# Kernel tuning notes

Measured on AMD Instinct MI355X. Metric: run time of the kernel, lower is better.

The kernel has to match this reference:

```python
import jax, jax.numpy as jnp
import numpy as np

B, C, N = 2, 32, 1_000_000
V = 262_144  # num_voxels (64^3 grid)


def setup_inputs() -> dict:
    key = jax.random.key(0)
    kf, ki = jax.random.split(key)
    features = jax.random.normal(kf, (B, C, N), dtype=jnp.float32)
    indices = jax.random.randint(ki, (N,), 0, V, dtype=jnp.int32)
    return {"features": features, "indices": indices, "num_voxels": V}


def reference(features, indices, num_voxels):
    # voxelize: scatter-mean over irregular cluster indices (dim=2)
    b, c, n = features.shape
    sums = jnp.zeros((b, c, num_voxels), dtype=features.dtype).at[:, :, indices].add(features)
    counts = jnp.zeros((num_voxels,), dtype=features.dtype).at[indices].add(1.0)
    voxels = sums / jnp.maximum(counts, 1.0)  # [B, C, V]; empty voxels -> 0
    # devoxelize: gather voxel features back to points via the same index buffer
    points_out = voxels[:, :, indices]  # [B, C, N]
    return points_out
```

## Files before the change

### kernel.cpp

```cpp
#include <hip/hip_runtime.h>


constexpr int BC  = 64;
constexpr int VOX = 262144;
constexpr int SCAN_BLK = 1024;
constexpr int NSB = VOX / SCAN_BLK;
constexpr int RV  = 128;

__global__ __launch_bounds__(256) void hist_kernel(
    const int* __restrict__ idx, int* __restrict__ cursor, int N)
{
    int t = blockIdx.x * 256 + threadIdx.x;
    int n0 = t * 4;
    if (n0 >= N) return;
    int4 vi = *(const int4*)(idx + n0);
    atomicAdd(&cursor[vi.x], 1);
    atomicAdd(&cursor[vi.y], 1);
    atomicAdd(&cursor[vi.z], 1);
    atomicAdd(&cursor[vi.w], 1);
}

__global__ __launch_bounds__(256) void scan_blocks(
    int* __restrict__ cursor, int* __restrict__ partials)
{
    __shared__ int sm[256];
    int t = threadIdx.x, b = blockIdx.x;
    int base = b * SCAN_BLK + t * 4;
    int4 c = *(const int4*)(cursor + base);
    int s = c.x + c.y + c.z + c.w;
    sm[t] = s;
    __syncthreads();
    #pragma unroll
    for (int off = 1; off < 256; off <<= 1) {
        int add = (t >= off) ? sm[t - off] : 0;
        __syncthreads();
        sm[t] += add;
        __syncthreads();
    }
    int excl = sm[t] - s;
    int4 o;
    o.x = excl; o.y = excl + c.x; o.z = o.y + c.y; o.w = o.z + c.z;
    *(int4*)(cursor + base) = o;
    if (t == 255) partials[b] = sm[255];
}

__global__ __launch_bounds__(256) void scan_partials(int* __restrict__ partials)
{
    __shared__ int sm[256];
    int t = threadIdx.x;
    int v = partials[t];
    sm[t] = v;
    __syncthreads();
    #pragma unroll
    for (int off = 1; off < 256; off <<= 1) {
        int add = (t >= off) ? sm[t - off] : 0;
        __syncthreads();
        sm[t] += add;
        __syncthreads();
    }
    partials[t] = sm[t] - v;
}

__global__ __launch_bounds__(256) void scan_add(
    int* __restrict__ cursor, const int* __restrict__ partials)
{
    int t = blockIdx.x * 256 + threadIdx.x;
    int base = t * 4;
    int add = partials[base >> 10];
    int4 c = *(int4*)(cursor + base);
    c.x += add; c.y += add; c.z += add; c.w += add;
    *(int4*)(cursor + base) = c;
}

__global__ __launch_bounds__(256) void permute_scatter(
    const float* __restrict__ feat, const int* __restrict__ idx,
    int* __restrict__ cursor, float* __restrict__ sorted, int N)
{
    int p = blockIdx.x * 256 + threadIdx.x;
    if (p >= N) return;
    int v = idx[p];
    int j = atomicAdd(&cursor[v], 1);
    float* dst = sorted + (size_t)j * BC;

    #pragma unroll
    for (int c0 = 0; c0 < BC; c0 += 16) {
        float f[16];
        #pragma unroll
        for (int k = 0; k < 16; ++k)
            f[k] = feat[(size_t)(c0 + k) * N + p];
        #pragma unroll
        for (int q = 0; q < 4; ++q)
            *(float4*)(dst + c0 + 4 * q) =
                make_float4(f[4*q], f[4*q+1], f[4*q+2], f[4*q+3]);
    }
}

__global__ __launch_bounds__(256) void reduce_mean(
    const float* __restrict__ sorted, const int* __restrict__ cursor,
    float* __restrict__ mean)
{
    int t = threadIdx.x;
    int vL = t & (RV - 1);
    int half = t >> 7;
    int v = blockIdx.x * RV + vL;

    int end = cursor[v];
    int start = (v > 0) ? cursor[v - 1] : 0;
    float inv = 1.0f / fmaxf((float)(end - start), 1.0f);

    float4 acc[8] = {};
    for (int j = start; j < end; ++j) {
        const float4* row = (const float4*)(sorted + (size_t)j * BC) + half * 8;
        #pragma unroll
        for (int q = 0; q < 8; ++q) {
            float4 r = row[q];
            acc[q].x += r.x; acc[q].y += r.y; acc[q].z += r.z; acc[q].w += r.w;
        }
    }
    float* dst = mean + (size_t)v * BC + half * 32;
    #pragma unroll
    for (int q = 0; q < 8; ++q) {
        float4 o = make_float4(acc[q].x * inv, acc[q].y * inv,
                               acc[q].z * inv, acc[q].w * inv);
        *(float4*)(dst + 4 * q) = o;
    }
}

__global__ __launch_bounds__(256) void voxel_gather(
    const float* __restrict__ mean, const int* __restrict__ idx,
    float* __restrict__ out, int N)
{
    int p = blockIdx.x * 256 + threadIdx.x;
    if (p >= N) return;
    int v = idx[p];
    const float4* row = (const float4*)(mean + (size_t)v * BC);
    #pragma unroll
    for (int q = 0; q < 16; ++q) {
        float4 r = row[q];
        __builtin_nontemporal_store(r.x, &out[(size_t)(4 * q + 0) * N + p]);
        __builtin_nontemporal_store(r.y, &out[(size_t)(4 * q + 1) * N + p]);
        __builtin_nontemporal_store(r.z, &out[(size_t)(4 * q + 2) * N + p]);
        __builtin_nontemporal_store(r.w, &out[(size_t)(4 * q + 3) * N + p]);
    }
}

extern "C" void kernel_launch(void* const* d_in, const int* in_sizes, int n_in,
                              void* d_out, int out_size, void* d_ws, size_t ws_size,
                              hipStream_t stream) {
    const float* feat = (const float*)d_in[0];
    const int* idx = (const int*)d_in[1];
    float* out = (float*)d_out;
    int N = in_sizes[1];

    float* mean = (float*)d_ws;
    int* cursor = (int*)((char*)d_ws + (size_t)VOX * BC * 4);
    int* partials = (int*)d_ws;
    float* sorted = (float*)d_out;

    hipMemsetAsync(cursor, 0, (size_t)VOX * sizeof(int), stream);

    int pblocks4 = ((N + 3) / 4 + 255) / 256;
    int pblocks1 = (N + 255) / 256;

    hist_kernel    <<<pblocks4, 256, 0, stream>>>(idx, cursor, N);
    scan_blocks    <<<NSB, 256, 0, stream>>>(cursor, partials);
    scan_partials  <<<1, 256, 0, stream>>>(partials);
    scan_add       <<<VOX / SCAN_BLK, 256, 0, stream>>>(cursor, partials);
    permute_scatter<<<pblocks1, 256, 0, stream>>>(feat, idx, cursor, sorted, N);
    reduce_mean    <<<VOX / RV, 256, 0, stream>>>(sorted, cursor, mean);
    voxel_gather   <<<pblocks1, 256, 0, stream>>>(mean, idx, out, N);
}
```

Before: 781.6 us.

## Use wave-per-voxel coalesced reduction and LDS-staged gather transpose

```diff
diff --git a/kernel.cpp b/kernel.cpp
--- a/kernel.cpp
+++ b/kernel.cpp
@@ -5,7 +5,7 @@
 constexpr int VOX = 262144;
 constexpr int SCAN_BLK = 1024;
 constexpr int NSB = VOX / SCAN_BLK;
-constexpr int RV  = 128;
+constexpr int WV  = 8;
 
 __global__ __launch_bounds__(256) void hist_kernel(
     const int* __restrict__ idx, int* __restrict__ cursor, int N)
@@ -87,7 +87,7 @@
         float f[16];
         #pragma unroll
         for (int k = 0; k < 16; ++k)
-            f[k] = feat[(size_t)(c0 + k) * N + p];
+            f[k] = __builtin_nontemporal_load(&feat[(size_t)(c0 + k) * N + p]);
         #pragma unroll
         for (int q = 0; q < 4; ++q)
             *(float4*)(dst + c0 + 4 * q) =
@@ -99,30 +99,20 @@
     const float* __restrict__ sorted, const int* __restrict__ cursor,
     float* __restrict__ mean)
 {
-    int t = threadIdx.x;
-    int vL = t & (RV - 1);
-    int half = t >> 7;
-    int v = blockIdx.x * RV + vL;
+    int wave = (blockIdx.x * 256 + threadIdx.x) >> 6;
+    int lane = threadIdx.x & 63;
+    int v0 = wave * WV;
 
-    int end = cursor[v];
-    int start = (v > 0) ? cursor[v - 1] : 0;
-    float inv = 1.0f / fmaxf((float)(end - start), 1.0f);
-
-    float4 acc[8] = {};
-    for (int j = start; j < end; ++j) {
-        const float4* row = (const float4*)(sorted + (size_t)j * BC) + half * 8;
-        #pragma unroll
-        for (int q = 0; q < 8; ++q) {
-            float4 r = row[q];
-            acc[q].x += r.x; acc[q].y += r.y; acc[q].z += r.z; acc[q].w += r.w;
-        }
-    }
-    float* dst = mean + (size_t)v * BC + half * 32;
-    #pragma unroll
-    for (int q = 0; q < 8; ++q) {
-        float4 o = make_float4(acc[q].x * inv, acc[q].y * inv,
-                               acc[q].z * inv, acc[q].w * inv);
-        *(float4*)(dst + 4 * q) = o;
+    int start = (v0 > 0) ? cursor[v0 - 1] : 0;
+    for (int i = 0; i < WV; ++i) {
+        int v = v0 + i;
+        int end = cursor[v];
+        float acc = 0.f;
+        for (int j = start; j < end; ++j)
+            acc += sorted[(size_t)j * BC + lane];
+        float inv = 1.0f / fmaxf((float)(end - start), 1.0f);
+        mean[(size_t)v * BC + lane] = acc * inv;
+        start = end;
     }
 }
 
@@ -130,17 +120,28 @@
     const float* __restrict__ mean, const int* __restrict__ idx,
     float* __restrict__ out, int N)
 {
-    int p = blockIdx.x * 256 + threadIdx.x;
-    if (p >= N) return;
-    int v = idx[p];
-    const float4* row = (const float4*)(mean + (size_t)v * BC);
-    #pragma unroll
-    for (int q = 0; q < 16; ++q) {
-        float4 r = row[q];
-        __builtin_nontemporal_store(r.x, &out[(size_t)(4 * q + 0) * N + p]);
-        __builtin_nontemporal_store(r.y, &out[(size_t)(4 * q + 1) * N + p]);
-        __builtin_nontemporal_store(r.z, &out[(size_t)(4 * q + 2) * N + p]);
-        __builtin_nontemporal_store(r.w, &out[(size_t)(4 * q + 3) * N + p]);
+    __shared__ float tile[256][BC + 1];
+    int tid = threadIdx.x;
+    int wave = tid >> 6, lane = tid & 63;
+    int p0 = blockIdx.x * 256;
+
+    int wbase = p0 + wave * 64;
+    int wcount = N - wbase;
+    if (wcount > 64) wcount = 64;
+
+    int pme = wbase + lane;
+    int vme = (pme < N) ? idx[pme] : 0;
+    for (int i = 0; i < wcount; ++i) {
+        int v = __shfl(vme, i);
+        tile[wave * 64 + i][lane] = mean[(size_t)v * BC + lane];
+    }
+    __syncthreads();
+
+    int p = p0 + tid;
+    if (p < N) {
+        #pragma unroll
+        for (int c = 0; c < BC; ++c)
+            __builtin_nontemporal_store(tile[tid][c], &out[(size_t)c * N + p]);
     }
 }
 
@@ -167,6 +168,6 @@
     scan_partials  <<<1, 256, 0, stream>>>(partials);
     scan_add       <<<VOX / SCAN_BLK, 256, 0, stream>>>(cursor, partials);
     permute_scatter<<<pblocks1, 256, 0, stream>>>(feat, idx, cursor, sorted, N);
-    reduce_mean    <<<VOX / RV, 256, 0, stream>>>(sorted, cursor, mean);
+    reduce_mean    <<<VOX / (WV * 4), 256, 0, stream>>>(sorted, cursor, mean);
     voxel_gather   <<<pblocks1, 256, 0, stream>>>(mean, idx, out, N);
 }
```

New measurement: 887.3 us. 13.5% more time.
